# Performance work log

Measured on AMD Instinct MI355X. Metric: run time of the kernel, lower is better.

## Reference

```python
import jax, jax.numpy as jnp
import numpy as np

B, S, HID = 16, 1024, 768
NH, HD = 12, 64  # num_heads, head_dim


def setup_inputs() -> dict:
    key = jax.random.key(0)
    ks = jax.random.split(key, 10)
    s = 0.02
    return {
        "hidden_states": jax.random.normal(ks[0], (B, S, HID), jnp.float32),
        "channel_importance": jnp.ones((HID,), jnp.float32),
        "context_importance": jnp.ones((HID,), jnp.float32),
        # Linear weights stored as (in, out): y = x @ W + b (== torch x @ W_t.T + b)
        "Wq": jax.random.normal(ks[1], (HID, HID), jnp.float32) * s,
        "bq": jnp.zeros((HID,), jnp.float32),
        "Wk": jax.random.normal(ks[2], (HID, HID), jnp.float32) * s,
        "bk": jnp.zeros((HID,), jnp.float32),
        "Wv": jax.random.normal(ks[3], (HID, HID), jnp.float32) * s,
        "bv": jnp.zeros((HID,), jnp.float32),
        "Wo": jax.random.normal(ks[4], (HID, HID), jnp.float32) * s,
        "bo": jnp.zeros((HID,), jnp.float32),
    }


def reference(hidden_states, channel_importance, context_importance,
              Wq, bq, Wk, bk, Wv, bv, Wo, bo):
    # channel-importance scaling (prune=False branch skipped)
    h = hidden_states * channel_importance  # [B,S,HID]
    # Q/K/V projections, split into heads: [B,S,HID] -> [B,NH,S,HD]
    def heads(x):
        return x.reshape(B, S, NH, HD).transpose(0, 2, 1, 3)
    q = heads(h @ Wq + bq)
    k = heads(h @ Wk + bk)
    v = heads(h @ Wv + bv)
    # scaled dot-product attention (dropout rate 0 -> identity)
    scores = jnp.einsum('bhqd,bhkd->bhqk', q, k) / jnp.sqrt(jnp.float32(HD))
    probs = jax.nn.softmax(scores, axis=-1)
    ctx = jnp.einsum('bhqk,bhkd->bhqd', probs, v)
    ctx = ctx.transpose(0, 2, 1, 3).reshape(B, S, HID)
    # context channel-importance scaling, then output projection
    ctx = ctx * context_importance
    out = ctx @ Wo + bo
    return out  # weights=None since visualize=False
```

## Files before the change

kernel.cpp:

```cpp
#include <hip/hip_runtime.h>
#include <hip/hip_bf16.h>

typedef unsigned short u16;
typedef short bf16x8 __attribute__((ext_vector_type(8)));
typedef float f32x4 __attribute__((ext_vector_type(4)));
typedef float f32x16 __attribute__((ext_vector_type(16)));
typedef unsigned short u16x4 __attribute__((ext_vector_type(4)));
typedef unsigned u32x4 __attribute__((ext_vector_type(4)));

#define SCALE_Q 0.18033688011112042f

__device__ __forceinline__ u16 f2b(float f) {
    __hip_bfloat16 h = __float2bfloat16(f);
    return *reinterpret_cast<u16*>(&h);
}

__device__ __forceinline__ unsigned cvt_pk_bf16(float lo, float hi) {
    unsigned r;
    asm("v_cvt_pk_bf16_f32 %0, %1, %2" : "=v"(r) : "v"(lo), "v"(hi));
    return r;
}

#define hw_exp2 __builtin_amdgcn_exp2f
#define hw_rcp  __builtin_amdgcn_rcpf

__device__ __forceinline__ void load_lds16(const void* g, void* l) {
    __builtin_amdgcn_global_load_lds(
        (const __attribute__((address_space(1))) void*)g,
        (__attribute__((address_space(3))) void*)l, 16, 0, 0);
}

__global__ __launch_bounds__(256) void prep_hidden(
    const float* __restrict__ x, const float* __restrict__ ci, u16* __restrict__ hbuf) {
    size_t i = ((size_t)blockIdx.x * 256 + threadIdx.x) * 4;
    float4 v = *(const float4*)(x + i);
    int c = (int)(i % 768);
    u16x4 o;
    o.x = f2b(v.x * ci[c]);     o.y = f2b(v.y * ci[c + 1]);
    o.z = f2b(v.z * ci[c + 2]); o.w = f2b(v.w * ci[c + 3]);
    *(u16x4*)(hbuf + i) = o;
}

__global__ __launch_bounds__(256) void transpose_w(
    const float* __restrict__ Wq, const float* __restrict__ Wk,
    const float* __restrict__ Wv, const float* __restrict__ Wo,
    const float* __restrict__ cc, u16* __restrict__ wqkvt, u16* __restrict__ wot) {
    __shared__ float tile[32][33];
    int z = blockIdx.z;
    const float* src = (z == 0) ? Wq : (z == 1) ? Wk : (z == 2) ? Wv : Wo;
    u16* dst = (z < 3) ? (wqkvt + (size_t)z * 768 * 768) : wot;
    int tx = threadIdx.x & 31, ty = threadIdx.x >> 5;
    int k0 = blockIdx.x * 32, n0 = blockIdx.y * 32;
    #pragma unroll
    for (int i = ty; i < 32; i += 8) {
        float v = src[(size_t)(k0 + i) * 768 + n0 + tx];
        if (z == 3) v *= cc[k0 + i];
        if (z == 0) v *= SCALE_Q;
        tile[i][tx] = v;
    }
    __syncthreads();
    #pragma unroll
    for (int i = ty; i < 32; i += 8)
        dst[(size_t)(n0 + i) * 768 + k0 + tx] = f2b(tile[tx][i]);
}

__global__ __launch_bounds__(256) void bias_cat(
    const float* __restrict__ bq, const float* __restrict__ bk,
    const float* __restrict__ bv, float* __restrict__ biasq) {
    int i = blockIdx.x * 256 + threadIdx.x;
    biasq[i] = (i < 768) ? bq[i] * SCALE_Q : (i < 1536) ? bk[i - 768] : bv[i - 1536];
}

template <int F32OUT>
__global__ __launch_bounds__(256) void gemm_bt(
    const u16* __restrict__ A, const u16* __restrict__ Bt,
    const float* __restrict__ bias, void* __restrict__ Cout,
    int M, int N, int K, int NTN) {
    __shared__ u16 lA[128 * 64];
    __shared__ u16 lB[128 * 64];
    int nwg = gridDim.x;
    int bid = blockIdx.x;
    int wg = ((nwg & 7) == 0) ? ((bid & 7) * (nwg >> 3) + (bid >> 3)) : bid;
    int mt = wg / NTN, nt = wg % NTN;
    int row0 = mt << 7, col0 = nt << 7;
    int tid = threadIdx.x;
    int lane = tid & 63, wv = tid >> 6;
    int wm = (wv >> 1) * 64, wn = (wv & 1) * 64;
    int l15 = lane & 15, hi = lane >> 4;

    f32x4 acc[4][4] = {};

    for (int kt = 0; kt < K; kt += 64) {
        __syncthreads();
        #pragma unroll
        for (int p = 0; p < 4; ++p) {
            int cl = p * 256 + tid;
            int rr = cl >> 3;
            int cc = (cl & 7) ^ (rr & 7);
            int lo = (p * 256 + (wv << 6)) << 3;
            load_lds16(A + (size_t)(row0 + rr) * K + kt + cc * 8, &lA[lo]);
            load_lds16(Bt + (size_t)(col0 + rr) * K + kt + cc * 8, &lB[lo]);
        }
        __syncthreads();
        __builtin_amdgcn_s_setprio(1);
        #pragma unroll
        for (int ks = 0; ks < 2; ++ks) {
            bf16x8 af[4], bf[4];
            #pragma unroll
            for (int i = 0; i < 4; ++i) {
                int ra = wm + i * 16 + l15;
                af[i] = *(const bf16x8*)&lA[ra * 64 + (((ks << 2) + hi) ^ (ra & 7)) * 8];
                int rb = wn + i * 16 + l15;
                bf[i] = *(const bf16x8*)&lB[rb * 64 + (((ks << 2) + hi) ^ (rb & 7)) * 8];
            }
            #pragma unroll
            for (int mi = 0; mi < 4; ++mi)
                #pragma unroll
                for (int ni = 0; ni < 4; ++ni)
                    acc[mi][ni] = __builtin_amdgcn_mfma_f32_16x16x32_bf16(
                        af[mi], bf[ni], acc[mi][ni], 0, 0, 0);
        }
        __builtin_amdgcn_s_setprio(0);
    }

    #pragma unroll
    for (int mi = 0; mi < 4; ++mi) {
        int rbase = row0 + wm + mi * 16 + hi * 4;
        #pragma unroll
        for (int ni = 0; ni < 4; ++ni) {
            int c = col0 + wn + ni * 16 + l15;
            float bv = bias[c];
            #pragma unroll
            for (int j = 0; j < 4; ++j) {
                float o = acc[mi][ni][j] + bv;
                if (F32OUT) ((float*)Cout)[(size_t)(rbase + j) * N + c] = o;
                else        ((u16*)Cout)[(size_t)(rbase + j) * N + c] = f2b(o);
            }
        }
    }
}

__global__ __launch_bounds__(512, 4) void attn_kernel(
    const u16* __restrict__ QKV, u16* __restrict__ ctx) {
    __shared__ u16 lK[2][64 * 64];
    __shared__ u16 lV[2][64 * 68];

    int bid = blockIdx.x;
    int wg = (bid & 7) * 96 + (bid >> 3);
    int bh = wg >> 2, qt = wg & 3;
    int b = bh / 12, h = bh % 12;
    int tid = threadIdx.x;
    int lane = tid & 63, wv = tid >> 6;
    int l31 = lane & 31;
    int hb = lane >> 5;

    const u16* Qb = QKV + (size_t)b * 1024 * 2304 + h * 64;
    const u16* Kb = Qb + 768;
    const u16* Vb = Qb + 1536;

    int qrow0 = qt * 256 + wv * 32;

    bf16x8 qf[4];
    #pragma unroll
    for (int ks = 0; ks < 4; ++ks)
        qf[ks] = *(const bf16x8*)(Qb + (size_t)(qrow0 + l31) * 2304 + ks * 16 + hb * 8);

    f32x16 accO0 = {}, accO1 = {};
    float lacc = 0.f;

    int krr = tid >> 3;
    int kcc = (tid & 7) ^ (krr & 7);
    bool vstage = tid < 256;
    int jj0 = (tid & 31) * 2;
    int jjs = (jj0 & ~12) | ((jj0 & 4) << 1) | ((jj0 & 8) >> 1);
    int d0v = ((tid >> 5) & 7) << 3;

    load_lds16(Kb + (size_t)krr * 2304 + kcc * 8, &lK[0][(wv << 6) << 3]);
    if (vstage) {
        bf16x8 g0 = *(const bf16x8*)(Vb + (size_t)jj0 * 2304 + d0v);
        bf16x8 g1 = *(const bf16x8*)(Vb + (size_t)(jj0 + 1) * 2304 + d0v);
        const unsigned* a0 = (const unsigned*)&g0;
        const unsigned* a1 = (const unsigned*)&g1;
        #pragma unroll
        for (int w = 0; w < 4; ++w) {
            *(unsigned*)&lV[0][(d0v + 2 * w) * 68 + jjs] =
                __builtin_amdgcn_perm(a1[w], a0[w], 0x05040100);
            *(unsigned*)&lV[0][(d0v + 2 * w + 1) * 68 + jjs] =
                __builtin_amdgcn_perm(a1[w], a0[w], 0x07060302);
        }
    }
    __syncthreads();

    int cur = 0;
    for (int t = 0; t < 16; ++t) {
        bf16x8 nv0, nv1;
        if (t < 15) {
            size_t kt1 = (size_t)(t + 1) * 64;
            load_lds16(Kb + (kt1 + krr) * 2304 + kcc * 8, &lK[cur ^ 1][(wv << 6) << 3]);
            if (vstage) {
                nv0 = *(const bf16x8*)(Vb + (kt1 + jj0) * 2304 + d0v);
                nv1 = *(const bf16x8*)(Vb + (kt1 + jj0 + 1) * 2304 + d0v);
            }
        }

        #pragma unroll
        for (int kvb = 0; kvb < 2; ++kvb) {
            f32x16 accs = {};
            __builtin_amdgcn_s_setprio(1);
            #pragma unroll
            for (int ks = 0; ks < 4; ++ks) {
                bf16x8 kf = *(const bf16x8*)&lK[cur][
                    (kvb * 32 + l31) * 64 + (((ks << 1) + hb) ^ (l31 & 7)) * 8];
                accs = __builtin_amdgcn_mfma_f32_32x32x16_bf16(kf, qf[ks], accs, 0, 0, 0);
            }
            __builtin_amdgcn_s_setprio(0);

            unsigned W[8];
            float ls = 0.f;
            #pragma unroll
            for (int w = 0; w < 8; ++w) {
                float e0 = hw_exp2(accs[2 * w]);
                float e1 = hw_exp2(accs[2 * w + 1]);
                ls += e0 + e1;
                W[w] = cvt_pk_bf16(e0, e1);
            }
            lacc += ls;

            __builtin_amdgcn_s_setprio(1);
            #pragma unroll
            for (int mm = 0; mm < 2; ++mm) {
                int m = kvb * 2 + mm;
                u32x4 pw;
                pw.x = W[4 * mm];     pw.y = W[4 * mm + 1];
                pw.z = W[4 * mm + 2]; pw.w = W[4 * mm + 3];
                bf16x8 pa = *(bf16x8*)&pw;
                bf16x8 vf0 = *(const bf16x8*)&lV[cur][l31 * 68 + m * 16 + hb * 8];
                bf16x8 vf1 = *(const bf16x8*)&lV[cur][(32 + l31) * 68 + m * 16 + hb * 8];
                accO0 = __builtin_amdgcn_mfma_f32_32x32x16_bf16(pa, vf0, accO0, 0, 0, 0);
                accO1 = __builtin_amdgcn_mfma_f32_32x32x16_bf16(pa, vf1, accO1, 0, 0, 0);
            }
            __builtin_amdgcn_s_setprio(0);
        }

        if (t < 15 && vstage) {
            const unsigned* a0 = (const unsigned*)&nv0;
            const unsigned* a1 = (const unsigned*)&nv1;
            #pragma unroll
            for (int w = 0; w < 4; ++w) {
                *(unsigned*)&lV[cur ^ 1][(d0v + 2 * w) * 68 + jjs] =
                    __builtin_amdgcn_perm(a1[w], a0[w], 0x05040100);
                *(unsigned*)&lV[cur ^ 1][(d0v + 2 * w + 1) * 68 + jjs] =
                    __builtin_amdgcn_perm(a1[w], a0[w], 0x07060302);
            }
        }

        __syncthreads();
        cur ^= 1;
    }

    float lsum = lacc + __shfl_xor(lacc, 32);
    #pragma unroll
    for (int r = 0; r < 16; ++r) {
        int q = (r & 3) + 8 * (r >> 2) + hb * 4;
        float Lr = __shfl(lsum, q);
        float inv = hw_rcp(Lr);
        size_t row = (size_t)(b * 1024 + qrow0 + q);
        ctx[row * 768 + h * 64 + l31]      = f2b(accO0[r] * inv);
        ctx[row * 768 + h * 64 + 32 + l31] = f2b(accO1[r] * inv);
    }
}

extern "C" void kernel_launch(void* const* d_in, const int* in_sizes, int n_in,
                              void* d_out, int out_size, void* d_ws, size_t ws_size,
                              hipStream_t stream) {
    const float* x  = (const float*)d_in[0];
    const float* ci = (const float*)d_in[1];
    const float* cc = (const float*)d_in[2];
    const float* Wq = (const float*)d_in[3];
    const float* bq = (const float*)d_in[4];
    const float* Wk = (const float*)d_in[5];
    const float* bk = (const float*)d_in[6];
    const float* Wv = (const float*)d_in[7];
    const float* bv = (const float*)d_in[8];
    const float* Wo = (const float*)d_in[9];
    const float* bo = (const float*)d_in[10];
    float* out = (float*)d_out;

    unsigned char* ws = (unsigned char*)d_ws;
    size_t off = 0;
    auto alloc = [&](size_t bytes) {
        void* p = ws + off;
        off += (bytes + 255) & ~(size_t)255;
        return p;
    };
    u16*   hbuf  = (u16*)  alloc((size_t)16384 * 768 * 2);
    u16*   wqkvt = (u16*)  alloc((size_t)2304 * 768 * 2);
    u16*   wot   = (u16*)  alloc((size_t)768 * 768 * 2);
    float* biasq = (float*)alloc(2304 * 4);
    u16*   qkv   = (u16*)  alloc((size_t)16384 * 2304 * 2);
    u16*   ctx   = (u16*)  alloc((size_t)16384 * 768 * 2);

    prep_hidden<<<12288, 256, 0, stream>>>(x, ci, hbuf);
    transpose_w<<<dim3(24, 24, 4), 256, 0, stream>>>(Wq, Wk, Wv, Wo, cc, wqkvt, wot);
    bias_cat<<<9, 256, 0, stream>>>(bq, bk, bv, biasq);
    gemm_bt<0><<<2304, 256, 0, stream>>>(hbuf, wqkvt, biasq, qkv, 16384, 2304, 768, 18);
    attn_kernel<<<768, 512, 0, stream>>>(qkv, ctx);
    gemm_bt<1><<<768, 256, 0, stream>>>(ctx, wot, bo, out, 16384, 768, 768, 6);
}
```

Before: 180.4 us.

## Triple-buffer LDS in bf16 GEMM with 256x128 tiles and 8 waves

Rewrites the bt-GEMM used for the QKV and output projections to use 512-thread workgroups computing 256x128 output tiles. K-tiles are staged into a three-slot LDS ring with direct global-to-LDS loads issued two steps ahead, and explicit vmcnt/lgkmcnt waits plus barriers replace the old per-iteration double sync. The goal is to hide global load latency behind MFMA work and to reuse each B tile across more rows. In exchange the kernel uses about 147 KB of LDS, which limits each CU to one workgroup, and it relies on hand-counted waitcnt values being correct.

```diff
diff --git a/kernel.cpp b/kernel.cpp
--- a/kernel.cpp
+++ b/kernel.cpp
@@ -72,36 +72,46 @@
 }
 
 template <int F32OUT>
-__global__ __launch_bounds__(256) void gemm_bt(
+__global__ __launch_bounds__(512) void gemm_bt(
     const u16* __restrict__ A, const u16* __restrict__ Bt,
     const float* __restrict__ bias, void* __restrict__ Cout,
     int M, int N, int K, int NTN) {
-    __shared__ u16 lA[128 * 64];
-    __shared__ u16 lB[128 * 64];
+    __shared__ u16 lds[3 * 24576];
     int nwg = gridDim.x;
     int bid = blockIdx.x;
     int wg = ((nwg & 7) == 0) ? ((bid & 7) * (nwg >> 3) + (bid >> 3)) : bid;
     int mt = wg / NTN, nt = wg % NTN;
-    int row0 = mt << 7, col0 = nt << 7;
+    int row0 = mt << 8, col0 = nt << 7;
     int tid = threadIdx.x;
     int lane = tid & 63, wv = tid >> 6;
-    int wm = (wv >> 1) * 64, wn = (wv & 1) * 64;
+    int wm = (wv >> 1) << 6;
+    int wn = (wv & 1) << 6;
     int l15 = lane & 15, hi = lane >> 4;
 
     f32x4 acc[4][4] = {};
 
-    for (int kt = 0; kt < K; kt += 64) {
-        __syncthreads();
+    auto STAGE = [&](int kt, int s) {
+        u16* sl = &lds[s * 24576];
+        size_t kof = (size_t)kt << 6;
         #pragma unroll
         for (int p = 0; p < 4; ++p) {
-            int cl = p * 256 + tid;
-            int rr = cl >> 3;
-            int cc = (cl & 7) ^ (rr & 7);
-            int lo = (p * 256 + (wv << 6)) << 3;
-            load_lds16(A + (size_t)(row0 + rr) * K + kt + cc * 8, &lA[lo]);
-            load_lds16(Bt + (size_t)(col0 + rr) * K + kt + cc * 8, &lB[lo]);
-        }
-        __syncthreads();
+            int c = p * 512 + tid;
+            int rr = c >> 3, cc = (c & 7) ^ (rr & 7);
+            load_lds16(A + (size_t)(row0 + rr) * K + kof + cc * 8,
+                       &sl[(p * 512 + (wv << 6)) << 3]);
+        }
+        #pragma unroll
+        for (int p = 0; p < 2; ++p) {
+            int c = p * 512 + tid;
+            int rr = c >> 3, cc = (c & 7) ^ (rr & 7);
+            load_lds16(Bt + (size_t)(col0 + rr) * K + kof + cc * 8,
+                       &sl[16384 + ((p * 512 + (wv << 6)) << 3)]);
+        }
+    };
+
+    auto COMPUTE = [&](int s) {
+        u16* sA = &lds[s * 24576];
+        u16* sB = sA + 16384;
         __builtin_amdgcn_s_setprio(1);
         #pragma unroll
         for (int ks = 0; ks < 2; ++ks) {
@@ -109,9 +119,9 @@
             #pragma unroll
             for (int i = 0; i < 4; ++i) {
                 int ra = wm + i * 16 + l15;
-                af[i] = *(const bf16x8*)&lA[ra * 64 + (((ks << 2) + hi) ^ (ra & 7)) * 8];
+                af[i] = *(const bf16x8*)&sA[ra * 64 + (((ks << 2) + hi) ^ (ra & 7)) * 8];
                 int rb = wn + i * 16 + l15;
-                bf[i] = *(const bf16x8*)&lB[rb * 64 + (((ks << 2) + hi) ^ (rb & 7)) * 8];
+                bf[i] = *(const bf16x8*)&sB[rb * 64 + (((ks << 2) + hi) ^ (rb & 7)) * 8];
             }
             #pragma unroll
             for (int mi = 0; mi < 4; ++mi)
@@ -121,7 +131,32 @@
                         af[mi], bf[ni], acc[mi][ni], 0, 0, 0);
         }
         __builtin_amdgcn_s_setprio(0);
-    }
+    };
+
+    int nkt = K >> 6;
+    STAGE(0, 0);
+    STAGE(1, 1);
+
+    int s = 0;
+    for (int kt = 0; kt < nkt - 2; ++kt) {
+        int s2 = s + 2; if (s2 >= 3) s2 -= 3;
+        STAGE(kt + 2, s2);
+        asm volatile("s_waitcnt vmcnt(12)" ::: "memory");
+        __builtin_amdgcn_s_barrier();
+        COMPUTE(s);
+        asm volatile("s_waitcnt lgkmcnt(0)" ::: "memory");
+        __builtin_amdgcn_s_barrier();
+        if (++s == 3) s = 0;
+    }
+    asm volatile("s_waitcnt vmcnt(6)" ::: "memory");
+    __builtin_amdgcn_s_barrier();
+    COMPUTE(s);
+    asm volatile("s_waitcnt lgkmcnt(0)" ::: "memory");
+    __builtin_amdgcn_s_barrier();
+    if (++s == 3) s = 0;
+    asm volatile("s_waitcnt vmcnt(0)" ::: "memory");
+    __builtin_amdgcn_s_barrier();
+    COMPUTE(s);
 
     #pragma unroll
     for (int mi = 0; mi < 4; ++mi) {
@@ -303,7 +338,7 @@
     prep_hidden<<<12288, 256, 0, stream>>>(x, ci, hbuf);
     transpose_w<<<dim3(24, 24, 4), 256, 0, stream>>>(Wq, Wk, Wv, Wo, cc, wqkvt, wot);
     bias_cat<<<9, 256, 0, stream>>>(bq, bk, bv, biasq);
-    gemm_bt<0><<<2304, 256, 0, stream>>>(hbuf, wqkvt, biasq, qkv, 16384, 2304, 768, 18);
+    gemm_bt<0><<<1152, 512, 0, stream>>>(hbuf, wqkvt, biasq, qkv, 16384, 2304, 768, 18);
     attn_kernel<<<768, 512, 0, stream>>>(qkv, ctx);
-    gemm_bt<1><<<768, 256, 0, stream>>>(ctx, wot, bo, out, 16384, 768, 768, 6);
-}
+    gemm_bt<1><<<384, 512, 0, stream>>>(ctx, wot, bo, out, 16384, 768, 768, 6);
+}
```

After: 202.3 us. 12.2% more time.
